# Kernel optimization log

Measured on AMD Instinct MI355X. Metric: run time of the kernel, lower is better.

## Reference

```python
import jax, jax.numpy as jnp
import numpy as np

N = 100000
E = 1600000
D_IN = 128
D_HID = 128


def setup_inputs() -> dict:
    key = jax.random.key(0)
    ks = jax.random.split(key, 10)
    x = jax.random.normal(ks[0], (N, D_IN), dtype=jnp.float32)
    edge_index = jax.random.randint(ks[1], (2, E), 0, N, dtype=jnp.int64)
    def lin(k, i, o):
        kw, kb = jax.random.split(k)
        s = 1.0 / np.sqrt(i)
        return (jax.random.uniform(kw, (o, i), jnp.float32, -s, s),
                jax.random.uniform(kb, (o,), jnp.float32, -s, s))
    w0a, b0a = lin(ks[2], D_IN, D_HID)
    w0b, b0b = lin(ks[3], D_HID, D_HID)
    w1a, b1a = lin(ks[4], D_HID, D_HID)
    w1b, b1b = lin(ks[5], D_HID, D_HID)
    return {"x": x, "edge_index": edge_index,
            "w0a": w0a, "b0a": b0a, "w0b": w0b, "b0b": b0b,
            "w1a": w1a, "b1a": b1a, "w1b": w1b, "b1b": b1b}


def _gin_layer(x, src, dst, wa, ba, wb, bb):
    # GINConv, eps=0: h_i = x_i + sum_{j in N(i)} x_j (messages from src aggregated at dst)
    agg = jax.ops.segment_sum(x[src], dst, num_segments=N)  # [N, D]
    h = x + agg
    h = jax.nn.relu(h @ wa.T + ba)  # LinearBlock (no bn, no dropout)
    return h @ wb.T + bb            # final Linear of local_nn


def reference(x, edge_index, w0a, b0a, w0b, b0b, w1a, b1a, w1b, b1b):
    src, dst = edge_index[0], edge_index[1]
    h = _gin_layer(x, src, dst, w0a, b0a, w0b, b0b)
    h = _gin_layer(h, src, dst, w1a, b1a, w1b, b1b)
    return h
```

## Files before the change

kernel.cpp:

```cpp
#include <hip/hip_runtime.h>


typedef __attribute__((ext_vector_type(8))) short bf16x8;
typedef __attribute__((ext_vector_type(4))) float floatx4;
typedef __attribute__((ext_vector_type(2))) float floatx2;
typedef __attribute__((ext_vector_type(4))) unsigned uintx4;

#define WS_ALIGN(x) (((x) + 255) & ~(size_t)255)
#define NBMAX 400
#define BCAP 6144

__device__ __forceinline__ unsigned short f2b(float f) {
  unsigned u = __builtin_bit_cast(unsigned, f);
  u = (u + 0x7FFF + ((u >> 16) & 1)) >> 16;
  return (unsigned short)u;
}

__device__ __forceinline__ floatx2 bpair(unsigned d) {
  floatx2 r;
  r[0] = __builtin_bit_cast(float, d << 16);
  r[1] = __builtin_bit_cast(float, d & 0xffff0000u);
  return r;
}

__global__ __launch_bounds__(256) void bucket_split(const int* __restrict__ src,
                                                    const int* __restrict__ dst,
                                                    int* __restrict__ bcnt,
                                                    unsigned* __restrict__ barr, int E, int nb) {
  __shared__ int cnt[NBMAX], base[NBMAX], cur[NBMAX];
  int t = threadIdx.x;
  for (int i = t; i < nb; i += 256) { cnt[i] = 0; cur[i] = 0; }
  __syncthreads();
  int e0 = blockIdx.x * 8192;
  int s[32], d[32];
#pragma unroll
  for (int k = 0; k < 32; k++) {
    int e = e0 + k * 256 + t;
    if (e < E) { s[k] = src[e]; d[k] = dst[e]; } else { d[k] = -1; }
  }
#pragma unroll
  for (int k = 0; k < 32; k++)
    if (d[k] >= 0) atomicAdd(&cnt[d[k] >> 8], 1);
  __syncthreads();
  for (int i = t; i < nb; i += 256) base[i] = cnt[i] ? atomicAdd(&bcnt[i], cnt[i]) : 0;
  __syncthreads();
#pragma unroll
  for (int k = 0; k < 32; k++)
    if (d[k] >= 0) {
      int b = d[k] >> 8;
      int r = atomicAdd(&cur[b], 1);
      barr[(size_t)b * BCAP + base[b] + r] = ((unsigned)(d[k] & 255) << 17) | (unsigned)s[k];
    }
}

__global__ void bucket_scan(const int* __restrict__ bcnt, int* __restrict__ sbase, int nb,
                            int* __restrict__ rowptr, int n) {
  __shared__ int buf[512];
  int t = threadIdx.x;
  int v = (t < nb) ? (bcnt[t] + 1024) : 0;
  buf[t] = v;
  __syncthreads();
  for (int off = 1; off < 512; off <<= 1) {
    int add = (t >= off) ? buf[t - off] : 0;
    __syncthreads();
    buf[t] += add;
    __syncthreads();
  }
  if (t < nb) sbase[t] = buf[t] - v;
  if (t == nb - 1) { sbase[nb] = buf[t]; rowptr[n] = buf[t]; }
}

__global__ __launch_bounds__(256) void bucket_csr(const unsigned* __restrict__ barr,
                                                  const int* __restrict__ bcnt,
                                                  const int* __restrict__ sbase,
                                                  int* __restrict__ rowptr,
                                                  int* __restrict__ degp,
                                                  int* __restrict__ srt, int n) {
  __shared__ int cnt[256], off[256], off2[256];
  int b = blockIdx.x, t = threadIdx.x;
  int cb = bcnt[b];
  int node0 = b * 256;
  int nlocal = min(256, n - node0);
  cnt[t] = 0;
  off2[t] = 0;
  __syncthreads();
  const unsigned* bp = barr + (size_t)b * BCAP;
  for (int i = t; i < cb; i += 256) atomicAdd(&cnt[bp[i] >> 17], 1);
  __syncthreads();
  int v = cnt[t];
  int vp = (v + 4) & ~3;
  off[t] = vp;
  __syncthreads();
  for (int o = 1; o < 256; o <<= 1) {
    int add = (t >= o) ? off[t - o] : 0;
    __syncthreads();
    off[t] += add;
    __syncthreads();
  }
  int excl = off[t] - vp;
  int sb = sbase[b];
  if (t < nlocal) {
    rowptr[node0 + t] = sb + excl;
    degp[node0 + t] = vp;
  }
  cnt[t] = excl;
  __syncthreads();
  for (int i = t; i < cb; i += 256) {
    unsigned pk = bp[i];
    int local = pk >> 17;
    int r = atomicAdd(&off2[local], 1);
    srt[sb + cnt[local] + r] = pk & 0x1FFFF;
  }
  if (t < nlocal) {
    int base = sb + excl;
    srt[base + v] = node0 + t;
    for (int i = v + 1; i < vp; i++) srt[base + i] = n;
  }
}

__global__ void cvt_kernel(const float* __restrict__ x, unsigned short* __restrict__ xb, int n4) {
  int i = blockIdx.x * blockDim.x + threadIdx.x;
  if (i < n4) {
    float4 v = ((const float4*)x)[i];
    uint2 pk;
    pk.x = (unsigned)f2b(v.x) | ((unsigned)f2b(v.y) << 16);
    pk.y = (unsigned)f2b(v.z) | ((unsigned)f2b(v.w) << 16);
    ((uint2*)xb)[i] = pk;
  }
}

__global__ __launch_bounds__(256) void aggregate_bf16(const uintx4* __restrict__ Xv,
                                                      const int* __restrict__ rowptr,
                                                      const int* __restrict__ degp,
                                                      const int* __restrict__ srt,
                                                      unsigned* __restrict__ out, int n) {
  int w = blockIdx.x * 4 + (threadIdx.x >> 6);
  if (w >= n) return;
  int lane = threadIdx.x & 63;
  int c = lane & 15;
  int s = lane >> 4;

  int p0 = rowptr[w] + s;
  int trips = degp[w] >> 2;

  floatx2 acc2[4];
#pragma unroll
  for (int i = 0; i < 4; i++) acc2[i] = floatx2{0.f, 0.f};

#pragma unroll 4
  for (int i = 0; i < trips; i++) {
    int r = srt[p0 + 4 * i];
    uintx4 u = Xv[(size_t)r * 16 + c];
    acc2[0] += bpair(u.x);
    acc2[1] += bpair(u.y);
    acc2[2] += bpair(u.z);
    acc2[3] += bpair(u.w);
  }

#pragma unroll
  for (int i = 0; i < 4; i++) {
#pragma unroll
    for (int k = 0; k < 2; k++) {
      acc2[i][k] += __shfl_xor(acc2[i][k], 16, 64);
      acc2[i][k] += __shfl_xor(acc2[i][k], 32, 64);
    }
  }

  unsigned pk = (unsigned)f2b(acc2[s][0]) | ((unsigned)f2b(acc2[s][1]) << 16);
  out[(size_t)w * 64 + c * 4 + s] = pk;
}

__device__ __forceinline__ void stage_w(char* buf, const float* __restrict__ W, int t) {
  for (int idx = t; idx < 2048; idx += 512) {
    int nrow = idx >> 4, c = idx & 15;
    float4 a = ((const float4*)W)[idx * 2];
    float4 b = ((const float4*)W)[idx * 2 + 1];
    uint4 pk;
    pk.x = (unsigned)f2b(a.x) | ((unsigned)f2b(a.y) << 16);
    pk.y = (unsigned)f2b(a.z) | ((unsigned)f2b(a.w) << 16);
    pk.z = (unsigned)f2b(b.x) | ((unsigned)f2b(b.y) << 16);
    pk.w = (unsigned)f2b(b.z) | ((unsigned)f2b(b.w) << 16);
    *(uint4*)(buf + nrow * 256 + ((c ^ (nrow & 15)) << 4)) = pk;
  }
}

template <int OUT_BF16>
__global__ __launch_bounds__(512) void mlp_kernel(
    const unsigned short* __restrict__ A, const float* __restrict__ Wa,
    const float* __restrict__ ba, const float* __restrict__ Wb,
    const float* __restrict__ bb, void* __restrict__ Cout, int n) {
  __shared__ __align__(16) char lds[65536];
  char* bufA = lds;
  char* bufB = lds + 32768;
  int t = threadIdx.x;
  stage_w(bufA, Wa, t);
  stage_w(bufB, Wb, t);

  int wave = t >> 6, lane = t & 63;
  int m = lane & 15, q = lane >> 4;
  int rbase = blockIdx.x * 128;
  int rowA = rbase + wave * 16 + m;
  int rA = rowA < n ? rowA : (n - 1);

  bf16x8 af[4];
  const bf16x8* Arow = (const bf16x8*)(A + (size_t)rA * 128);
#pragma unroll
  for (int ks = 0; ks < 4; ks++) af[ks] = Arow[ks * 4 + q];

  __syncthreads();

  floatx4 acc[8];
  floatx4 zf = {0.f, 0.f, 0.f, 0.f};
#pragma unroll
  for (int j = 0; j < 8; j++) acc[j] = zf;
#pragma unroll
  for (int ks = 0; ks < 4; ks++) {
#pragma unroll
    for (int j = 0; j < 8; j++) {
      bf16x8 bf = *(const bf16x8*)(bufA + (j * 16 + m) * 256 + (((ks * 4 + q) ^ m) << 4));
      acc[j] = __builtin_amdgcn_mfma_f32_16x16x32_bf16(af[ks], bf, acc[j], 0, 0, 0);
    }
  }
  __syncthreads();

#pragma unroll
  for (int j = 0; j < 8; j++) {
    float bias = ba[j * 16 + m];
#pragma unroll
    for (int reg = 0; reg < 4; reg++) {
      float v = fmaxf(acc[j][reg] + bias, 0.f);
      int lr = wave * 16 + q * 4 + reg;
      int col = j * 16 + m;
      *(unsigned short*)(bufA + lr * 256 + (((col >> 3) ^ (lr & 15)) << 4) + (col & 7) * 2) =
          f2b(v);
    }
  }
  __syncthreads();

  int lrA = wave * 16 + m;
#pragma unroll
  for (int ks = 0; ks < 4; ks++)
    af[ks] = *(const bf16x8*)(bufA + lrA * 256 + (((ks * 4 + q) ^ m) << 4));
#pragma unroll
  for (int j = 0; j < 8; j++) acc[j] = zf;
#pragma unroll
  for (int ks = 0; ks < 4; ks++) {
#pragma unroll
    for (int j = 0; j < 8; j++) {
      bf16x8 bf = *(const bf16x8*)(bufB + (j * 16 + m) * 256 + (((ks * 4 + q) ^ m) << 4));
      acc[j] = __builtin_amdgcn_mfma_f32_16x16x32_bf16(af[ks], bf, acc[j], 0, 0, 0);
    }
  }

#pragma unroll
  for (int j = 0; j < 8; j++) {
    float bias = bb[j * 16 + m];
#pragma unroll
    for (int reg = 0; reg < 4; reg++) {
      int row = rbase + wave * 16 + q * 4 + reg;
      if (row >= n) continue;
      float v = acc[j][reg] + bias;
      int col = j * 16 + m;
      if (OUT_BF16)
        ((unsigned short*)Cout)[(size_t)row * 128 + col] = f2b(v);
      else
        ((float*)Cout)[(size_t)row * 128 + col] = v;
    }
  }
}

extern "C" void kernel_launch(void* const* d_in, const int* in_sizes, int n_in,
                              void* d_out, int out_size, void* d_ws, size_t ws_size,
                              hipStream_t stream) {
  const float* x   = (const float*)d_in[0];
  const int*   ei  = (const int*)d_in[1];
  const float* w0a = (const float*)d_in[2];
  const float* b0a = (const float*)d_in[3];
  const float* w0b = (const float*)d_in[4];
  const float* b0b = (const float*)d_in[5];
  const float* w1a = (const float*)d_in[6];
  const float* b1a = (const float*)d_in[7];
  const float* w1b = (const float*)d_in[8];
  const float* b1b = (const float*)d_in[9];
  float* out = (float*)d_out;

  int n = in_sizes[0] / 128;
  int E = in_sizes[1] / 2;
  const int* src = ei;
  const int* dst = ei + E;
  int nb = (n + 255) / 256;

  char* w = (char*)d_ws;
  int* rowptr = (int*)w;           w += WS_ALIGN((size_t)(n + 1) * 4);
  int* sbase = (int*)w;            w += WS_ALIGN((size_t)(NBMAX + 1) * 4);
  int* bcnt = (int*)w;             w += WS_ALIGN((size_t)NBMAX * 4);
  int* degp = (int*)w;             w += WS_ALIGN((size_t)n * 4);
  int* srt = (int*)w;              w += WS_ALIGN(((size_t)E + NBMAX * 1024 + 1024) * 4);
  unsigned short* xb = (unsigned short*)w;  w += WS_ALIGN((size_t)(n + 1) * 128 * 2);
  unsigned* barr = (unsigned*)w;
  unsigned short* B1 = (unsigned short*)w;

  hipMemsetAsync(bcnt, 0, (size_t)nb * 4, stream);
  hipMemsetAsync(xb + (size_t)n * 128, 0, 256, stream);
  bucket_split<<<(E + 8191) / 8192, 256, 0, stream>>>(src, dst, bcnt, barr, E, nb);
  bucket_scan<<<1, 512, 0, stream>>>(bcnt, sbase, nb, rowptr, n);
  bucket_csr<<<nb, 256, 0, stream>>>(barr, bcnt, sbase, rowptr, degp, srt, n);

  cvt_kernel<<<(n * 32 + 255) / 256, 256, 0, stream>>>(x, xb, n * 32);

  int agg_grid = (n + 3) / 4;
  int mlp_grid = (n + 127) / 128;

  aggregate_bf16<<<agg_grid, 256, 0, stream>>>((const uintx4*)xb, rowptr, degp, srt,
                                               (unsigned*)B1, n);
  mlp_kernel<1><<<mlp_grid, 512, 0, stream>>>(B1, w0a, b0a, w0b, b0b, xb, n);

  aggregate_bf16<<<agg_grid, 256, 0, stream>>>((const uintx4*)xb, rowptr, degp, srt,
                                               (unsigned*)B1, n);
  mlp_kernel<0><<<mlp_grid, 512, 0, stream>>>(B1, w1a, b1a, w1b, b1b, out, n);
}
```

Baseline: 340.6 us.

## Split aggregation into feature halves with 8-way edge parallelism; preconvert weights once

The aggregation kernel now runs two blocks per group of nodes, each handling half of the 128 features. Each wave processes 8 neighbor rows in parallel with 8 lanes per row instead of 4 rows with 16 lanes. To support this, the CSR padding is raised to multiples of 8 and the slack in the sort buffer is enlarged. The four weight matrices are converted to bf16 once by a small kernel, so every MLP block copies the ready bf16 weights into LDS instead of converting them itself. The changes aim to expose more memory-level parallelism in the gather and to cut redundant conversion work. The cost is more padding entries, an extra shuffle-reduction step, and twice as many index loads.

```diff
diff --git a/kernel.cpp b/kernel.cpp
--- a/kernel.cpp
+++ b/kernel.cpp
@@ -57,7 +57,7 @@
                             int* __restrict__ rowptr, int n) {
   __shared__ int buf[512];
   int t = threadIdx.x;
-  int v = (t < nb) ? (bcnt[t] + 1024) : 0;
+  int v = (t < nb) ? (bcnt[t] + 2048) : 0;
   buf[t] = v;
   __syncthreads();
   for (int off = 1; off < 512; off <<= 1) {
@@ -88,7 +88,7 @@
   for (int i = t; i < cb; i += 256) atomicAdd(&cnt[bp[i] >> 17], 1);
   __syncthreads();
   int v = cnt[t];
-  int vp = (v + 4) & ~3;
+  int vp = (v + 8) & ~7;
   off[t] = vp;
   __syncthreads();
   for (int o = 1; o < 256; o <<= 1) {
@@ -129,28 +129,49 @@
   }
 }
 
+__global__ __launch_bounds__(256) void wcvt_kernel(const float* __restrict__ w0,
+                                                   const float* __restrict__ w1,
+                                                   const float* __restrict__ w2,
+                                                   const float* __restrict__ w3,
+                                                   uintx4* __restrict__ out) {
+  int i = blockIdx.x * 256 + threadIdx.x;
+  const float* W = (i < 2048) ? w0 : (i < 4096) ? w1 : (i < 6144) ? w2 : w3;
+  int j = i & 2047;
+  float4 a = ((const float4*)W)[j * 2];
+  float4 b = ((const float4*)W)[j * 2 + 1];
+  uintx4 pk;
+  pk.x = (unsigned)f2b(a.x) | ((unsigned)f2b(a.y) << 16);
+  pk.y = (unsigned)f2b(a.z) | ((unsigned)f2b(a.w) << 16);
+  pk.z = (unsigned)f2b(b.x) | ((unsigned)f2b(b.y) << 16);
+  pk.w = (unsigned)f2b(b.z) | ((unsigned)f2b(b.w) << 16);
+  out[i] = pk;
+}
+
 __global__ __launch_bounds__(256) void aggregate_bf16(const uintx4* __restrict__ Xv,
                                                       const int* __restrict__ rowptr,
                                                       const int* __restrict__ degp,
                                                       const int* __restrict__ srt,
                                                       unsigned* __restrict__ out, int n) {
-  int w = blockIdx.x * 4 + (threadIdx.x >> 6);
+  int b = blockIdx.x;
+  int h = b & 1;
+  int w = (b >> 1) * 4 + (threadIdx.x >> 6);
   if (w >= n) return;
   int lane = threadIdx.x & 63;
-  int c = lane & 15;
-  int s = lane >> 4;
+  int c = lane & 7;
+  int s = lane >> 3;
 
   int p0 = rowptr[w] + s;
-  int trips = degp[w] >> 2;
+  int trips = degp[w] >> 3;
+  const uintx4* Xh = Xv + (size_t)h * 8;
 
   floatx2 acc2[4];
 #pragma unroll
   for (int i = 0; i < 4; i++) acc2[i] = floatx2{0.f, 0.f};
 
-#pragma unroll 4
+#pragma unroll 2
   for (int i = 0; i < trips; i++) {
-    int r = srt[p0 + 4 * i];
-    uintx4 u = Xv[(size_t)r * 16 + c];
+    int r = srt[p0 + 8 * i];
+    uintx4 u = Xh[(size_t)r * 16 + c];
     acc2[0] += bpair(u.x);
     acc2[1] += bpair(u.y);
     acc2[2] += bpair(u.z);
@@ -161,40 +182,37 @@
   for (int i = 0; i < 4; i++) {
 #pragma unroll
     for (int k = 0; k < 2; k++) {
+      acc2[i][k] += __shfl_xor(acc2[i][k], 8, 64);
       acc2[i][k] += __shfl_xor(acc2[i][k], 16, 64);
       acc2[i][k] += __shfl_xor(acc2[i][k], 32, 64);
     }
   }
 
-  unsigned pk = (unsigned)f2b(acc2[s][0]) | ((unsigned)f2b(acc2[s][1]) << 16);
-  out[(size_t)w * 64 + c * 4 + s] = pk;
-}
-
-__device__ __forceinline__ void stage_w(char* buf, const float* __restrict__ W, int t) {
+  if (s < 4) {
+    unsigned pk = (unsigned)f2b(acc2[s][0]) | ((unsigned)f2b(acc2[s][1]) << 16);
+    out[(size_t)w * 64 + h * 32 + c * 4 + s] = pk;
+  }
+}
+
+__device__ __forceinline__ void stage_wb(char* buf, const uintx4* __restrict__ Wb, int t) {
   for (int idx = t; idx < 2048; idx += 512) {
     int nrow = idx >> 4, c = idx & 15;
-    float4 a = ((const float4*)W)[idx * 2];
-    float4 b = ((const float4*)W)[idx * 2 + 1];
-    uint4 pk;
-    pk.x = (unsigned)f2b(a.x) | ((unsigned)f2b(a.y) << 16);
-    pk.y = (unsigned)f2b(a.z) | ((unsigned)f2b(a.w) << 16);
-    pk.z = (unsigned)f2b(b.x) | ((unsigned)f2b(b.y) << 16);
-    pk.w = (unsigned)f2b(b.z) | ((unsigned)f2b(b.w) << 16);
-    *(uint4*)(buf + nrow * 256 + ((c ^ (nrow & 15)) << 4)) = pk;
+    uintx4 pk = Wb[idx];
+    *(uintx4*)(buf + nrow * 256 + ((c ^ (nrow & 15)) << 4)) = pk;
   }
 }
 
 template <int OUT_BF16>
 __global__ __launch_bounds__(512) void mlp_kernel(
-    const unsigned short* __restrict__ A, const float* __restrict__ Wa,
-    const float* __restrict__ ba, const float* __restrict__ Wb,
+    const unsigned short* __restrict__ A, const uintx4* __restrict__ Wa16,
+    const float* __restrict__ ba, const uintx4* __restrict__ Wb16,
     const float* __restrict__ bb, void* __restrict__ Cout, int n) {
   __shared__ __align__(16) char lds[65536];
   char* bufA = lds;
   char* bufB = lds + 32768;
   int t = threadIdx.x;
-  stage_w(bufA, Wa, t);
-  stage_w(bufB, Wb, t);
+  stage_wb(bufA, Wa16, t);
+  stage_wb(bufB, Wb16, t);
 
   int wave = t >> 6, lane = t & 63;
   int m = lane & 15, q = lane >> 4;
@@ -295,8 +313,9 @@
   int* sbase = (int*)w;            w += WS_ALIGN((size_t)(NBMAX + 1) * 4);
   int* bcnt = (int*)w;             w += WS_ALIGN((size_t)NBMAX * 4);
   int* degp = (int*)w;             w += WS_ALIGN((size_t)n * 4);
-  int* srt = (int*)w;              w += WS_ALIGN(((size_t)E + NBMAX * 1024 + 1024) * 4);
+  int* srt = (int*)w;              w += WS_ALIGN(((size_t)E + NBMAX * 2048 + 1024) * 4);
   unsigned short* xb = (unsigned short*)w;  w += WS_ALIGN((size_t)(n + 1) * 128 * 2);
+  uintx4* wb16 = (uintx4*)w;       w += WS_ALIGN((size_t)8192 * 16);
   unsigned* barr = (unsigned*)w;
   unsigned short* B1 = (unsigned short*)w;
 
@@ -306,16 +325,18 @@
   bucket_scan<<<1, 512, 0, stream>>>(bcnt, sbase, nb, rowptr, n);
   bucket_csr<<<nb, 256, 0, stream>>>(barr, bcnt, sbase, rowptr, degp, srt, n);
 
+  wcvt_kernel<<<32, 256, 0, stream>>>(w0a, w0b, w1a, w1b, wb16);
+
   cvt_kernel<<<(n * 32 + 255) / 256, 256, 0, stream>>>(x, xb, n * 32);
 
-  int agg_grid = (n + 3) / 4;
+  int agg_grid = ((n + 3) / 4) * 2;
   int mlp_grid = (n + 127) / 128;
 
   aggregate_bf16<<<agg_grid, 256, 0, stream>>>((const uintx4*)xb, rowptr, degp, srt,
                                                (unsigned*)B1, n);
-  mlp_kernel<1><<<mlp_grid, 512, 0, stream>>>(B1, w0a, b0a, w0b, b0b, xb, n);
+  mlp_kernel<1><<<mlp_grid, 512, 0, stream>>>(B1, wb16, b0a, wb16 + 2048, b0b, xb, n);
 
   aggregate_bf16<<<agg_grid, 256, 0, stream>>>((const uintx4*)xb, rowptr, degp, srt,
                                                (unsigned*)B1, n);
-  mlp_kernel<0><<<mlp_grid, 512, 0, stream>>>(B1, w1a, b1a, w1b, b1b, out, n);
-}
+  mlp_kernel<0><<<mlp_grid, 512, 0, stream>>>(B1, wb16 + 4096, b1a, wb16 + 6144, b1b, out, n);
+}
```

Measured after the change: 370.2 us. +8.7%, slower.
